# Kernel optimization log

Measured on AMD Instinct MI355X. Metric: run time of the kernel, lower is better.

The kernel has to match this reference:

```python
import jax, jax.numpy as jnp
import numpy as np

D = 256; H = 8; DH = D // H; L = 4; P = 4; NADJ = 4; DFF = 1024
SPATIAL_SHAPES = [(100, 134), (50, 67), (25, 34), (13, 17)]
LEVEL_START = [0, 13400, 16750, 17600]
LV = 17821
B, NQ, NP = 4, 100, 20


def layer_norm(x, g, b, eps=1e-5):
    m = x.mean(-1, keepdims=True)
    v = ((x - m) ** 2).mean(-1, keepdims=True)
    return (x - m) / jnp.sqrt(v + eps) * g + b


def mha(q, k, v, wi, bi, wo, bo):
    # q,k,v: [B', S, D]; torch nn.MultiheadAttention math (eval, no attn dropout effect on expectation pathway matters only in train)
    d = q.shape[-1]
    qp = q @ wi[:d].T + bi[:d]
    kp = k @ wi[d:2 * d].T + bi[d:2 * d]
    vp = v @ wi[2 * d:].T + bi[2 * d:]
    Bq, S, _ = qp.shape
    sp = lambda t: t.reshape(Bq, -1, H, DH).transpose(0, 2, 1, 3)
    att = jax.nn.softmax(jnp.einsum('bhqd,bhkd->bhqk', sp(qp), sp(kp)) / (DH ** 0.5), axis=-1)
    o = jnp.einsum('bhqk,bhkd->bhqd', att, sp(vp)).transpose(0, 2, 1, 3).reshape(Bq, S, d)
    return o @ wo.T + bo


def circonv(x, cw, cb, g, b, m, v):
    # Conv1d over point dim with circular padding NADJ, then BatchNorm1d (eval stats) + ReLU
    Bx, Nq, Np, d = x.shape
    t = x.reshape(Bx * Nq, Np, d).transpose(0, 2, 1)  # [B*Nq, C, Np]
    t = jnp.concatenate([t[..., -NADJ:], t, t[..., :NADJ]], axis=-1)
    t = jax.lax.conv_general_dilated(t, cw, (1,), 'VALID', dimension_numbers=('NCH', 'OIH', 'NCH'))
    t = t + cb[None, :, None]
    t = (t - m[None, :, None]) / jnp.sqrt(v[None, :, None] + 1e-5) * g[None, :, None] + b[None, :, None]
    t = jax.nn.relu(t)
    return t.transpose(0, 2, 1).reshape(Bx, Nq, Np, d)


def bilinear_gather(vflat, Hl, Wl, x, y):
    # vflat: [NB, Hl*Wl, DH]; x,y: [NB, S] pixel coords (align_corners=False, zero padding)
    x0 = jnp.floor(x); y0 = jnp.floor(y)
    lx = x - x0; ly = y - y0
    x0i = x0.astype(jnp.int32); y0i = y0.astype(jnp.int32)
    out = 0.
    for dy, wy in ((0, 1. - ly), (1, ly)):
        for dx, wx in ((0, 1. - lx), (1, lx)):
            xi = x0i + dx; yi = y0i + dy
            valid = (xi >= 0) & (xi < Wl) & (yi >= 0) & (yi < Hl)
            idx = jnp.clip(yi, 0, Hl - 1) * Wl + jnp.clip(xi, 0, Wl - 1)
            gs = jnp.take_along_axis(vflat, idx[..., None], axis=1)
            out = out + gs * (wx * wy * valid)[..., None]
    return out


def ms_deform_core(value, loc, weights):
    # value: [N, Lv, H, DH]; loc: [N, Lq, H, L, P, 2] in [0,1]; weights: [N, Lq, H, L, P]
    N, Lq = loc.shape[:2]
    out = jnp.zeros((N, Lq, H, DH), value.dtype)
    for lvl, (Hl, Wl) in enumerate(SPATIAL_SHAPES):
        s = LEVEL_START[lvl]
        vflat = value[:, s:s + Hl * Wl].transpose(0, 2, 1, 3).reshape(N * H, Hl * Wl, DH)
        g = 2. * loc[:, :, :, lvl] - 1.
        x = ((g[..., 0] + 1.) / 2.) * Wl - 0.5
        y = ((g[..., 1] + 1.) / 2.) * Hl - 0.5
        x = x.transpose(0, 2, 1, 3).reshape(N * H, Lq * P)
        y = y.transpose(0, 2, 1, 3).reshape(N * H, Lq * P)
        samp = bilinear_gather(vflat, Hl, Wl, x, y).reshape(N, H, Lq, P, DH)
        w = weights[:, :, :, lvl].transpose(0, 2, 1, 3)  # [N, H, Lq, P]
        out = out + jnp.einsum('nhqp,nhqpd->nqhd', w, samp)
    return out.reshape(N, Lq, D)


def ms_deform_attn(query, ref, src, so_w, so_b, aw_w, aw_b, vp_w, vp_b, op_w, op_b):
    N, Lq, _ = query.shape
    value = (src @ vp_w.T + vp_b).reshape(N, -1, H, DH)
    offsets = (query @ so_w.T + so_b).reshape(N, Lq, H, L, P, 2)
    aw = jax.nn.softmax((query @ aw_w.T + aw_b).reshape(N, Lq, H, L * P), -1).reshape(N, Lq, H, L, P)
    normalizer = jnp.array([[wl, hl] for hl, wl in SPATIAL_SHAPES], jnp.float32)  # [L, 2] (W, H)
    loc = ref[:, :, None, :, None, :] + offsets / normalizer[None, None, None, :, None, :]
    return ms_deform_core(value, loc, aw) @ op_w.T + op_b


def _forward(tgt, query_pos, query_pos_anchor, reference_points, src,
             ia_wi, ia_bi, ia_wo, ia_bo,
             cc_w, cc_b, bn_g, bn_b, bn_m, bn_v,
             ni_g, ni_b, mf_w, mf_b, nf_g, nf_b,
             in_wi, in_bi, in_wo, in_bo, nin_g, nin_b,
             so_w, so_b, aw_w, aw_b, vp_w, vp_b, op_w, op_b, nc_g, nc_b,
             l1_w, l1_b, l2_w, l2_b, n3_g, n3_b):
    Bx, Nq, Np, d = tgt.shape
    shortcut = tgt
    # intra-attention over points (DropPath/dropout are identity in eval)
    q = (tgt + query_pos).reshape(Bx * Nq, Np, d)
    t = mha(q, q, tgt.reshape(Bx * Nq, Np, d), ia_wi, ia_bi, ia_wo, ia_bo).reshape(Bx, Nq, Np, d)
    t_cc = circonv(shortcut + query_pos, cc_w, cc_b, bn_g, bn_b, bn_m, bn_v)
    tgt = shortcut + layer_norm(t + t_cc, ni_g, ni_b)
    tgt = tgt + layer_norm(tgt @ mf_w.T + mf_b, nf_g, nf_b)
    # inter-attention over instances
    ti = jnp.swapaxes(tgt, 1, 2)                                    # [B, Np, Nq, d]
    qi = jnp.swapaxes(tgt + query_pos_anchor, 1, 2).reshape(Bx * Np, Nq, d)
    t2 = mha(qi, qi, ti.reshape(Bx * Np, Nq, d), in_wi, in_bi, in_wo, in_bo).reshape(Bx, Np, Nq, d)
    ti = jnp.swapaxes(layer_norm(ti + t2, nin_g, nin_b), 1, 2)      # [B, Nq, Np, d]
    # deformable cross-attention
    qc = (ti + query_pos).reshape(Bx, Nq * Np, d)
    ref = reference_points.reshape(Bx, Nq * Np, L, 2)
    t2 = ms_deform_attn(qc, ref, src, so_w, so_b, aw_w, aw_b, vp_w, vp_b, op_w, op_b).reshape(Bx, Nq, Np, d)
    tgt = layer_norm(ti + t2, nc_g, nc_b)
    # FFN
    t2 = jax.nn.relu(tgt @ l1_w.T + l1_b) @ l2_w.T + l2_b
    return layer_norm(tgt + t2, n3_g, n3_b)


def setup_inputs() -> dict:
    ks = iter(jax.random.split(jax.random.key(0), 64))
    nx = lambda: next(ks)
    nrm = lambda shp, s=0.02: jax.random.normal(nx(), shp, jnp.float32) * s
    z = lambda shp: jnp.zeros(shp, jnp.float32)
    o = lambda shp: jnp.ones(shp, jnp.float32)
    inp = {
        'tgt': jax.random.normal(nx(), (B, NQ, NP, D), jnp.float32),
        'query_pos': jax.random.normal(nx(), (B, NQ, NP, D), jnp.float32),
        'query_pos_anchor': jax.random.normal(nx(), (B, NQ, NP, D), jnp.float32),
        'reference_points': jax.random.uniform(nx(), (B, NQ, NP, L, 2), jnp.float32),
        'src': jax.random.normal(nx(), (B, LV, D), jnp.float32),
        'src_spatial_shapes': jnp.array(SPATIAL_SHAPES, jnp.int32),
        'level_start_index': jnp.array(LEVEL_START, jnp.int32),
        'ia_wi': nrm((3 * D, D)), 'ia_bi': z((3 * D,)), 'ia_wo': nrm((D, D)), 'ia_bo': z((D,)),
        'cc_w': nrm((D, D, 2 * NADJ + 1), 0.01), 'cc_b': z((D,)),
        'bn_g': o((D,)), 'bn_b': z((D,)), 'bn_m': z((D,)), 'bn_v': o((D,)),
        'ni_g': o((D,)), 'ni_b': z((D,)),
        'mf_w': nrm((D, D)), 'mf_b': z((D,)),
        'nf_g': o((D,)), 'nf_b': z((D,)),
        'in_wi': nrm((3 * D, D)), 'in_bi': z((3 * D,)), 'in_wo': nrm((D, D)), 'in_bo': z((D,)),
        'nin_g': o((D,)), 'nin_b': z((D,)),
        'so_w': nrm((H * L * P * 2, D)), 'so_b': nrm((H * L * P * 2,), 0.1),
        'aw_w': nrm((H * L * P, D)), 'aw_b': z((H * L * P,)),
        'vp_w': nrm((D, D)), 'vp_b': z((D,)),
        'op_w': nrm((D, D)), 'op_b': z((D,)),
        'nc_g': o((D,)), 'nc_b': z((D,)),
        'l1_w': nrm((DFF, D)), 'l1_b': z((DFF,)),
        'l2_w': nrm((D, DFF)), 'l2_b': z((D,)),
        'n3_g': o((D,)), 'n3_b': z((D,)),
    }
    return inp


def reference(tgt, query_pos, query_pos_anchor, reference_points, src,
              src_spatial_shapes, level_start_index,
              ia_wi, ia_bi, ia_wo, ia_bo,
              cc_w, cc_b, bn_g, bn_b, bn_m, bn_v,
              ni_g, ni_b, mf_w, mf_b, nf_g, nf_b,
              in_wi, in_bi, in_wo, in_bo, nin_g, nin_b,
              so_w, so_b, aw_w, aw_b, vp_w, vp_b, op_w, op_b, nc_g, nc_b,
              l1_w, l1_b, l2_w, l2_b, n3_g, n3_b):
    # spatial shapes / level starts are compile-time constants (SPATIAL_SHAPES); the int tensors are accepted for API parity
    return _forward(tgt, query_pos, query_pos_anchor, reference_points, src,
                    ia_wi, ia_bi, ia_wo, ia_bo,
                    cc_w, cc_b, bn_g, bn_b, bn_m, bn_v,
                    ni_g, ni_b, mf_w, mf_b, nf_g, nf_b,
                    in_wi, in_bi, in_wo, in_bo, nin_g, nin_b,
                    so_w, so_b, aw_w, aw_b, vp_w, vp_b, op_w, op_b, nc_g, nc_b,
                    l1_w, l1_b, l2_w, l2_b, n3_g, n3_b)
```

## Files before the change

kernel.cpp:

```cpp
#include <hip/hip_runtime.h>
#include <cmath>

#define NTOK 8000
#define LV_TOT 17821

typedef __attribute__((ext_vector_type(8))) short short8;
typedef __attribute__((ext_vector_type(4))) float f32x4;

__device__ inline unsigned short f2bf(float f) {
  unsigned u = __float_as_uint(f);
  u += 0x7fffu + ((u >> 16) & 1u);
  return (unsigned short)(u >> 16);
}
__device__ inline short8 pack8(float4 a, float4 b) {
  short8 r;
  r[0] = (short)f2bf(a.x); r[1] = (short)f2bf(a.y);
  r[2] = (short)f2bf(a.z); r[3] = (short)f2bf(a.w);
  r[4] = (short)f2bf(b.x); r[5] = (short)f2bf(b.y);
  r[6] = (short)f2bf(b.z); r[7] = (short)f2bf(b.w);
  return r;
}
__device__ inline int swz(int row, int ib) {
  int s = ((ib >> 4) ^ (row & 3) ^ ((row >> 2) & 3)) & 3;
  return row * 64 + (s << 4) + (ib & 15);
}

__global__ __launch_bounds__(256) void add_kernel(const float* __restrict__ a,
                                                  const float* __restrict__ b,
                                                  float* __restrict__ o, int n4) {
  int i = blockIdx.x * 256 + threadIdx.x;
  if (i < n4) {
    float4 x = reinterpret_cast<const float4*>(a)[i];
    float4 y = reinterpret_cast<const float4*>(b)[i];
    float4 z; z.x = x.x + y.x; z.y = x.y + y.y; z.z = x.z + y.z; z.w = x.w + y.w;
    reinterpret_cast<float4*>(o)[i] = z;
  }
}

__global__ __launch_bounds__(256) void gemm_mfma_kernel(
    const float* __restrict__ A, const float* __restrict__ W,
    const float* __restrict__ s1, const float* __restrict__ s2,
    float* __restrict__ C, int M, int N, int K, int mode, int conv)
{
  __shared__ __align__(16) char lds[12288];
  char* ldsA = lds;
  char* ldsB = lds + 8192;

  const int tid = threadIdx.x;
  const int ar = tid >> 1, ac = (tid & 1) << 4;
  const int br = tid >> 2, bc = (tid & 3) << 3;
  const int arowg = blockIdx.y * 128 + ar;
  const int wrowg = blockIdx.x * 64 + br;
  const bool aval = arowg < M;
  int aseq = 0, anp = 0;
  if (conv) { aseq = arowg / 20; anp = arowg - aseq * 20; }
  const float* wsrc = W + (size_t)wrowg * K + bc;

  const int wv = tid >> 6, l = tid & 63, lr = l & 15, lk = l >> 4;

  f32x4 acc[2][4];
  #pragma unroll
  for (int m = 0; m < 2; ++m)
    #pragma unroll
    for (int n = 0; n < 4; ++n) acc[m][n] = (f32x4){0.f, 0.f, 0.f, 0.f};

  for (int k0 = 0; k0 < K; k0 += 32) {
    float4 a0 = make_float4(0.f,0.f,0.f,0.f), a1 = a0, a2 = a0, a3 = a0;
    if (aval) {
      const float* as;
      if (conv) {
        int kcol = k0 + ac, kt = kcol >> 8, c = kcol & 255;
        int sr = aseq * 20 + ((anp + kt + 16) % 20);
        as = A + (size_t)sr * 256 + c;
      } else {
        as = A + (size_t)arowg * K + k0 + ac;
      }
      a0 = *(const float4*)as;       a1 = *(const float4*)(as + 4);
      a2 = *(const float4*)(as + 8); a3 = *(const float4*)(as + 12);
    }
    float4 w0 = *(const float4*)(wsrc + k0);
    float4 w1 = *(const float4*)(wsrc + k0 + 4);
    __syncthreads();
    *(short8*)(ldsA + swz(ar, ac * 2))      = pack8(a0, a1);
    *(short8*)(ldsA + swz(ar, ac * 2 + 16)) = pack8(a2, a3);
    *(short8*)(ldsB + swz(br, bc * 2))      = pack8(w0, w1);
    __syncthreads();
    short8 af0 = *(short8*)(ldsA + swz(wv * 32 + lr,      lk * 16));
    short8 af1 = *(short8*)(ldsA + swz(wv * 32 + 16 + lr, lk * 16));
    #pragma unroll
    for (int n = 0; n < 4; ++n) {
      short8 bfr = *(short8*)(ldsB + swz(n * 16 + lr, lk * 16));
      acc[0][n] = __builtin_amdgcn_mfma_f32_16x16x32_bf16(af0, bfr, acc[0][n], 0, 0, 0);
      acc[1][n] = __builtin_amdgcn_mfma_f32_16x16x32_bf16(af1, bfr, acc[1][n], 0, 0, 0);
    }
  }
  #pragma unroll
  for (int n = 0; n < 4; ++n) {
    int gcol = blockIdx.x * 64 + n * 16 + lr;
    float sa = s1[gcol];
    float sb = (mode == 2) ? s2[gcol] : 0.f;
    #pragma unroll
    for (int m = 0; m < 2; ++m) {
      #pragma unroll
      for (int i = 0; i < 4; ++i) {
        int grow = blockIdx.y * 128 + wv * 32 + m * 16 + lk * 4 + i;
        if (grow < M) {
          float v = acc[m][n][i];
          v = (mode == 2) ? fmaxf(v * sa + sb, 0.f)
                          : (mode == 1 ? fmaxf(v + sa, 0.f) : v + sa);
          C[(size_t)grow * N + gcol] = v;
        }
      }
    }
  }
}

__global__ __launch_bounds__(256) void convw_kernel(const float* __restrict__ w,
                                                    float* __restrict__ w2) {
  int i = blockIdx.x * 256 + threadIdx.x;
  int o = i / 2304; int r = i - o * 2304;
  int k = r >> 8, c = r & 255;
  w2[i] = w[(size_t)o * 2304 + c * 9 + k];
}

__global__ __launch_bounds__(256) void bnfold_kernel(
    const float* __restrict__ cb, const float* __restrict__ g,
    const float* __restrict__ b,  const float* __restrict__ m,
    const float* __restrict__ v,  float* __restrict__ scale,
    float* __restrict__ shift) {
  int o = threadIdx.x;
  float s = g[o] * rsqrtf(v[o] + 1e-5f);
  scale[o] = s;
  shift[o] = (cb[o] - m[o]) * s + b[o];
}

__global__ __launch_bounds__(256) void ln_kernel(const float* __restrict__ x1,
    const float* __restrict__ x2, const float* __restrict__ x3,
    const float* __restrict__ g, const float* __restrict__ bta,
    float* __restrict__ out)
{
  int wid = threadIdx.x >> 6, lane = threadIdx.x & 63;
  size_t t = (size_t)blockIdx.x * 4 + wid;
  size_t base = t * 256 + (size_t)lane * 4;
  float4 v = *reinterpret_cast<const float4*>(x1 + base);
  if (x2) {
    float4 u = *reinterpret_cast<const float4*>(x2 + base);
    v.x += u.x; v.y += u.y; v.z += u.z; v.w += u.w;
  }
  float s  = v.x + v.y + v.z + v.w;
  float ss = v.x*v.x + v.y*v.y + v.z*v.z + v.w*v.w;
  #pragma unroll
  for (int off = 32; off; off >>= 1) {
    s  += __shfl_xor(s, off, 64);
    ss += __shfl_xor(ss, off, 64);
  }
  float mean = s * (1.0f / 256.0f);
  float var  = ss * (1.0f / 256.0f) - mean * mean;
  float rstd = rsqrtf(var + 1e-5f);
  float4 gv = *reinterpret_cast<const float4*>(g + lane * 4);
  float4 bv = *reinterpret_cast<const float4*>(bta + lane * 4);
  float4 o;
  o.x = (v.x - mean) * rstd * gv.x + bv.x;
  o.y = (v.y - mean) * rstd * gv.y + bv.y;
  o.z = (v.z - mean) * rstd * gv.z + bv.z;
  o.w = (v.w - mean) * rstd * gv.w + bv.w;
  if (x3) {
    float4 u = *reinterpret_cast<const float4*>(x3 + base);
    o.x += u.x; o.y += u.y; o.z += u.z; o.w += u.w;
  }
  *reinterpret_cast<float4*>(out + base) = o;
}

__global__ __launch_bounds__(256) void attn_intra_kernel(
    const float* __restrict__ qp, const float* __restrict__ kp,
    const float* __restrict__ vp, float* __restrict__ outb)
{
  __shared__ float Qs[20][257], Ks[20][257], Vs[20][257];
  int seq = blockIdx.x, t0 = seq * 20;
  for (int idx = threadIdx.x; idx < 20 * 256; idx += 256) {
    int r = idx >> 8, d = idx & 255;
    size_t g = (size_t)(t0 + r) * 256 + d;
    Qs[r][d] = qp[g]; Ks[r][d] = kp[g]; Vs[r][d] = vp[g];
  }
  __syncthreads();
  int h = threadIdx.x >> 5, i = threadIdx.x & 31;
  if (i < 20) {
    const float scale = 0.17677669529663687f;
    float s[20]; float m = -1e30f;
    #pragma unroll
    for (int j = 0; j < 20; ++j) {
      float a = 0.f;
      #pragma unroll
      for (int d = 0; d < 32; ++d) a += Qs[i][h*32+d] * Ks[j][h*32+d];
      a *= scale; s[j] = a; m = fmaxf(m, a);
    }
    float sum = 0.f;
    #pragma unroll
    for (int j = 0; j < 20; ++j) { s[j] = expf(s[j] - m); sum += s[j]; }
    float inv = 1.f / sum;
    #pragma unroll
    for (int d = 0; d < 32; ++d) {
      float o = 0.f;
      #pragma unroll
      for (int j = 0; j < 20; ++j) o += s[j] * Vs[j][h*32+d];
      outb[(size_t)(t0 + i) * 256 + h*32 + d] = o * inv;
    }
  }
}

__global__ __launch_bounds__(128) void attn_inter_kernel(
    const float* __restrict__ qp, const float* __restrict__ kp,
    const float* __restrict__ vp, float* __restrict__ outb)
{
  __shared__ float Ks[100][32], Vs[100][32];
  int blk = blockIdx.x;
  int h = blk & 7; int sp = blk >> 3; int np = sp % 20; int b = sp / 20;
  for (int idx = threadIdx.x; idx < 100 * 32; idx += 128) {
    int r = idx >> 5, d = idx & 31;
    size_t g = ((size_t)((b * 100 + r) * 20 + np)) * 256 + h*32 + d;
    Ks[r][d] = kp[g]; Vs[r][d] = vp[g];
  }
  __syncthreads();
  int i = threadIdx.x;
  if (i < 100) {
    size_t qbase = ((size_t)((b * 100 + i) * 20 + np)) * 256 + h*32;
    float q[32];
    #pragma unroll
    for (int d4 = 0; d4 < 8; ++d4) {
      float4 v = *reinterpret_cast<const float4*>(qp + qbase + d4*4);
      q[d4*4+0] = v.x; q[d4*4+1] = v.y; q[d4*4+2] = v.z; q[d4*4+3] = v.w;
    }
    const float scale = 0.17677669529663687f;
    float m = -1e30f, l = 0.f, o[32] = {};
    for (int j = 0; j < 100; ++j) {
      float s = 0.f;
      #pragma unroll
      for (int d = 0; d < 32; ++d) s += q[d] * Ks[j][d];
      s *= scale;
      float mn = fmaxf(m, s);
      float f = expf(m - mn), e = expf(s - mn);
      l = l * f + e;
      #pragma unroll
      for (int d = 0; d < 32; ++d) o[d] = o[d] * f + e * Vs[j][d];
      m = mn;
    }
    float inv = 1.f / l;
    #pragma unroll
    for (int d = 0; d < 32; ++d) outb[qbase + d] = o[d] * inv;
  }
}

__global__ __launch_bounds__(256) void deform_kernel(
    const float* __restrict__ value, const float* __restrict__ offs,
    const float* __restrict__ awl, const float* __restrict__ ref,
    float* __restrict__ outb)
{
  int t = blockIdx.x;
  int h = threadIdx.x >> 5, dh = threadIdx.x & 31;
  int b = t / 2000;
  float w[16]; float m = -1e30f;
  #pragma unroll
  for (int lp = 0; lp < 16; ++lp) {
    w[lp] = awl[(size_t)t * 128 + h * 16 + lp];
    m = fmaxf(m, w[lp]);
  }
  float sum = 0.f;
  #pragma unroll
  for (int lp = 0; lp < 16; ++lp) { w[lp] = expf(w[lp] - m); sum += w[lp]; }
  float inv = 1.f / sum;
  const int HLs[4] = {100, 50, 25, 13};
  const int WLs[4] = {134, 67, 34, 17};
  const int STs[4] = {0, 13400, 16750, 17600};
  float acc = 0.f;
  #pragma unroll
  for (int l = 0; l < 4; ++l) {
    const int Hl = HLs[l], Wl = WLs[l];
    const float* vb = value + ((size_t)(b * LV_TOT + STs[l])) * 256 + h*32 + dh;
    float rx = ref[(size_t)t * 8 + l * 2 + 0];
    float ry = ref[(size_t)t * 8 + l * 2 + 1];
    #pragma unroll
    for (int p = 0; p < 4; ++p) {
      size_t oi = (size_t)t * 256 + (size_t)(((h*4 + l)*4 + p)*2);
      float ox = offs[oi], oy = offs[oi + 1];
      float x = (rx + ox / (float)Wl) * (float)Wl - 0.5f;
      float y = (ry + oy / (float)Hl) * (float)Hl - 0.5f;
      float x0f = floorf(x), y0f = floorf(y);
      float lx = x - x0f, ly = y - y0f;
      int x0 = (int)x0f, y0 = (int)y0f;
      float wp = w[l*4 + p] * inv;
      float cw00 = (1.f-lx)*(1.f-ly)*wp, cw01 = lx*(1.f-ly)*wp;
      float cw10 = (1.f-lx)*ly*wp,       cw11 = lx*ly*wp;
      if (y0 >= 0 && y0 < Hl) {
        if (x0 >= 0 && x0 < Wl)         acc += cw00 * vb[(size_t)(y0*Wl + x0) * 256];
        if (x0+1 >= 0 && x0+1 < Wl)     acc += cw01 * vb[(size_t)(y0*Wl + x0+1) * 256];
      }
      if (y0+1 >= 0 && y0+1 < Hl) {
        if (x0 >= 0 && x0 < Wl)         acc += cw10 * vb[(size_t)((y0+1)*Wl + x0) * 256];
        if (x0+1 >= 0 && x0+1 < Wl)     acc += cw11 * vb[(size_t)((y0+1)*Wl + x0+1) * 256];
      }
    }
  }
  outb[(size_t)t * 256 + h*32 + dh] = acc;
}

extern "C" void kernel_launch(void* const* d_in, const int* in_sizes, int n_in,
                              void* d_out, int out_size, void* d_ws, size_t ws_size,
                              hipStream_t stream)
{
  const float* tgt  = (const float*)d_in[0];
  const float* qpos = (const float*)d_in[1];
  const float* qpa  = (const float*)d_in[2];
  const float* ref  = (const float*)d_in[3];
  const float* src  = (const float*)d_in[4];
  const float* ia_wi = (const float*)d_in[7];
  const float* ia_bi = (const float*)d_in[8];
  const float* ia_wo = (const float*)d_in[9];
  const float* ia_bo = (const float*)d_in[10];
  const float* cc_w  = (const float*)d_in[11];
  const float* cc_b  = (const float*)d_in[12];
  const float* bn_g  = (const float*)d_in[13];
  const float* bn_b  = (const float*)d_in[14];
  const float* bn_m  = (const float*)d_in[15];
  const float* bn_v  = (const float*)d_in[16];
  const float* ni_g  = (const float*)d_in[17];
  const float* ni_b  = (const float*)d_in[18];
  const float* mf_w  = (const float*)d_in[19];
  const float* mf_b  = (const float*)d_in[20];
  const float* nf_g  = (const float*)d_in[21];
  const float* nf_b  = (const float*)d_in[22];
  const float* in_wi = (const float*)d_in[23];
  const float* in_bi = (const float*)d_in[24];
  const float* in_wo = (const float*)d_in[25];
  const float* in_bo = (const float*)d_in[26];
  const float* nin_g = (const float*)d_in[27];
  const float* nin_b = (const float*)d_in[28];
  const float* so_w  = (const float*)d_in[29];
  const float* so_b  = (const float*)d_in[30];
  const float* aw_w  = (const float*)d_in[31];
  const float* aw_b  = (const float*)d_in[32];
  const float* vp_w  = (const float*)d_in[33];
  const float* vp_b  = (const float*)d_in[34];
  const float* op_w  = (const float*)d_in[35];
  const float* op_b  = (const float*)d_in[36];
  const float* nc_g  = (const float*)d_in[37];
  const float* nc_b  = (const float*)d_in[38];
  const float* l1_w  = (const float*)d_in[39];
  const float* l1_b  = (const float*)d_in[40];
  const float* l2_w  = (const float*)d_in[41];
  const float* l2_b  = (const float*)d_in[42];
  const float* n3_g  = (const float*)d_in[43];
  const float* n3_b  = (const float*)d_in[44];
  float* out = (float*)d_out;

  float* ws = (float*)d_ws;
  const size_t TD = (size_t)NTOK * 256;
  float* A   = ws;
  float* Bb  = ws + TD;
  float* Cc  = ws + 2*TD;
  float* Dd  = ws + 3*TD;
  float* Ee  = ws + 4*TD;
  float* V   = ws + 5*TD;
  float* W2  = V + (size_t)71284 * 256;
  float* bnscale = W2 + (size_t)256 * 2304;
  float* bnshift = bnscale + 256;
  float* Hbuf = V;

  dim3 blk(256);
  const int N4 = (int)(TD / 4);

  auto GEMM = [&](const float* Ain, const float* Win, const float* b1, const float* b2,
                  float* Cout, int M_, int N_, int K_, int mode, int conv) {
    dim3 g(N_ / 64, (M_ + 127) / 128);
    hipLaunchKernelGGL(gemm_mfma_kernel, g, blk, 0, stream,
                       Ain, Win, b1, b2, Cout, M_, N_, K_, mode, conv);
  };

  hipLaunchKernelGGL(add_kernel, dim3(2000), blk, 0, stream, tgt, qpos, A, N4);
  GEMM(A,   ia_wi,             ia_bi,       nullptr, Bb, NTOK, 256, 256, 0, 0);
  GEMM(A,   ia_wi + 256*256,   ia_bi + 256, nullptr, Cc, NTOK, 256, 256, 0, 0);
  GEMM(tgt, ia_wi + 512*256,   ia_bi + 512, nullptr, Dd, NTOK, 256, 256, 0, 0);
  hipLaunchKernelGGL(attn_intra_kernel, dim3(400), blk, 0, stream, Bb, Cc, Dd, Ee);
  GEMM(Ee,  ia_wo, ia_bo, nullptr, Bb, NTOK, 256, 256, 0, 0);

  hipLaunchKernelGGL(convw_kernel, dim3(2304), blk, 0, stream, cc_w, W2);
  hipLaunchKernelGGL(bnfold_kernel, dim3(1), blk, 0, stream,
                     cc_b, bn_g, bn_b, bn_m, bn_v, bnscale, bnshift);
  GEMM(A, W2, bnscale, bnshift, Cc, NTOK, 256, 2304, 2, 1);

  hipLaunchKernelGGL(ln_kernel, dim3(2000), blk, 0, stream, Bb, Cc, tgt, ni_g, ni_b, Dd);
  GEMM(Dd, mf_w, mf_b, nullptr, A, NTOK, 256, 256, 0, 0);
  hipLaunchKernelGGL(ln_kernel, dim3(2000), blk, 0, stream, A, (const float*)nullptr, Dd, nf_g, nf_b, Bb);

  hipLaunchKernelGGL(add_kernel, dim3(2000), blk, 0, stream, Bb, qpa, A, N4);
  GEMM(A,  in_wi,           in_bi,       nullptr, Cc, NTOK, 256, 256, 0, 0);
  GEMM(A,  in_wi + 256*256, in_bi + 256, nullptr, Dd, NTOK, 256, 256, 0, 0);
  GEMM(Bb, in_wi + 512*256, in_bi + 512, nullptr, Ee, NTOK, 256, 256, 0, 0);
  hipLaunchKernelGGL(attn_inter_kernel, dim3(640), dim3(128), 0, stream, Cc, Dd, Ee, A);
  GEMM(A, in_wo, in_bo, nullptr, Cc, NTOK, 256, 256, 0, 0);
  hipLaunchKernelGGL(ln_kernel, dim3(2000), blk, 0, stream, Bb, Cc, (const float*)nullptr, nin_g, nin_b, Dd);

  hipLaunchKernelGGL(add_kernel, dim3(2000), blk, 0, stream, Dd, qpos, A, N4);
  GEMM(src, vp_w, vp_b, nullptr, V, 4 * LV_TOT, 256, 256, 0, 0);
  GEMM(A, so_w, so_b, nullptr, Bb, NTOK, 256, 256, 0, 0);
  GEMM(A, aw_w, aw_b, nullptr, Cc, NTOK, 128, 256, 0, 0);
  hipLaunchKernelGGL(deform_kernel, dim3(NTOK), blk, 0, stream, V, Bb, Cc, ref, Ee);
  GEMM(Ee, op_w, op_b, nullptr, A, NTOK, 256, 256, 0, 0);
  hipLaunchKernelGGL(ln_kernel, dim3(2000), blk, 0, stream, Dd, A, (const float*)nullptr, nc_g, nc_b, Bb);

  GEMM(Bb, l1_w, l1_b, nullptr, Hbuf, NTOK, 1024, 256, 1, 0);
  GEMM(Hbuf, l2_w, l2_b, nullptr, A, NTOK, 256, 1024, 0, 0);
  hipLaunchKernelGGL(ln_kernel, dim3(2000), blk, 0, stream, Bb, A, (const float*)nullptr, n3_g, n3_b, out);
}
```

Measured before the change: 805.9 us.

## Fuse QKV projections, fold positional adds into GEMM loads, vectorize deform sampling

Merges the separate Q, K and V projection GEMMs into one GEMM with N=768, and merges the sampling-offset and attention-weight projections into one N=384 GEMM using a concatenated weight. The standalone add kernels are removed by adding the positional embedding during the GEMM A-tile load, applied only to column blocks below a limit. The deformable sampling kernel now runs four tokens per block, with each lane gathering float4 values. This cuts kernel launches and intermediate round trips, but the A operand is read twice when the add is active, and the new weight-concatenation kernel runs on every call.

```diff
diff --git a/kernel.cpp b/kernel.cpp
--- a/kernel.cpp
+++ b/kernel.cpp
@@ -25,22 +25,11 @@
   return row * 64 + (s << 4) + (ib & 15);
 }
 
-__global__ __launch_bounds__(256) void add_kernel(const float* __restrict__ a,
-                                                  const float* __restrict__ b,
-                                                  float* __restrict__ o, int n4) {
-  int i = blockIdx.x * 256 + threadIdx.x;
-  if (i < n4) {
-    float4 x = reinterpret_cast<const float4*>(a)[i];
-    float4 y = reinterpret_cast<const float4*>(b)[i];
-    float4 z; z.x = x.x + y.x; z.y = x.y + y.y; z.z = x.z + y.z; z.w = x.w + y.w;
-    reinterpret_cast<float4*>(o)[i] = z;
-  }
-}
-
 __global__ __launch_bounds__(256) void gemm_mfma_kernel(
-    const float* __restrict__ A, const float* __restrict__ W,
+    const float* __restrict__ A, const float* __restrict__ A2,
+    const float* __restrict__ W,
     const float* __restrict__ s1, const float* __restrict__ s2,
-    float* __restrict__ C, int M, int N, int K, int mode, int conv)
+    float* __restrict__ C, int M, int N, int K, int mode, int conv, int addLimit)
 {
   __shared__ __align__(16) char lds[12288];
   char* ldsA = lds;
@@ -52,6 +41,7 @@
   const int arowg = blockIdx.y * 128 + ar;
   const int wrowg = blockIdx.x * 64 + br;
   const bool aval = arowg < M;
+  const bool doadd = (A2 != nullptr) && ((int)blockIdx.x * 64 < addLimit);
   int aseq = 0, anp = 0;
   if (conv) { aseq = arowg / 20; anp = arowg - aseq * 20; }
   const float* wsrc = W + (size_t)wrowg * K + bc;
@@ -67,16 +57,26 @@
   for (int k0 = 0; k0 < K; k0 += 32) {
     float4 a0 = make_float4(0.f,0.f,0.f,0.f), a1 = a0, a2 = a0, a3 = a0;
     if (aval) {
-      const float* as;
+      size_t off;
       if (conv) {
         int kcol = k0 + ac, kt = kcol >> 8, c = kcol & 255;
         int sr = aseq * 20 + ((anp + kt + 16) % 20);
-        as = A + (size_t)sr * 256 + c;
+        off = (size_t)sr * 256 + c;
       } else {
-        as = A + (size_t)arowg * K + k0 + ac;
+        off = (size_t)arowg * K + k0 + ac;
       }
+      const float* as = A + off;
       a0 = *(const float4*)as;       a1 = *(const float4*)(as + 4);
       a2 = *(const float4*)(as + 8); a3 = *(const float4*)(as + 12);
+      if (doadd) {
+        const float* as2 = A2 + off;
+        float4 b0 = *(const float4*)as2;       float4 b1 = *(const float4*)(as2 + 4);
+        float4 b2 = *(const float4*)(as2 + 8); float4 b3 = *(const float4*)(as2 + 12);
+        a0.x+=b0.x; a0.y+=b0.y; a0.z+=b0.z; a0.w+=b0.w;
+        a1.x+=b1.x; a1.y+=b1.y; a1.z+=b1.z; a1.w+=b1.w;
+        a2.x+=b2.x; a2.y+=b2.y; a2.z+=b2.z; a2.w+=b2.w;
+        a3.x+=b3.x; a3.y+=b3.y; a3.z+=b3.z; a3.w+=b3.w;
+      }
     }
     float4 w0 = *(const float4*)(wsrc + k0);
     float4 w1 = *(const float4*)(wsrc + k0 + 4);
@@ -132,6 +132,15 @@
   float s = g[o] * rsqrtf(v[o] + 1e-5f);
   scale[o] = s;
   shift[o] = (cb[o] - m[o]) * s + b[o];
+}
+__global__ __launch_bounds__(256) void wcat_kernel(
+    const float* __restrict__ so_w, const float* __restrict__ so_b,
+    const float* __restrict__ aw_w, const float* __restrict__ aw_b,
+    float* __restrict__ wsb, float* __restrict__ bsb) {
+  int r = blockIdx.x, c = threadIdx.x;
+  wsb[(size_t)r * 256 + c] = (r < 256) ? so_w[(size_t)r * 256 + c]
+                                       : aw_w[(size_t)(r - 256) * 256 + c];
+  if (c == 0) bsb[r] = (r < 256) ? so_b[r] : aw_b[r - 256];
 }
 
 __global__ __launch_bounds__(256) void ln_kernel(const float* __restrict__ x1,
@@ -172,15 +181,14 @@
 }
 
 __global__ __launch_bounds__(256) void attn_intra_kernel(
-    const float* __restrict__ qp, const float* __restrict__ kp,
-    const float* __restrict__ vp, float* __restrict__ outb)
+    const float* __restrict__ qkv, float* __restrict__ outb)
 {
   __shared__ float Qs[20][257], Ks[20][257], Vs[20][257];
   int seq = blockIdx.x, t0 = seq * 20;
   for (int idx = threadIdx.x; idx < 20 * 256; idx += 256) {
     int r = idx >> 8, d = idx & 255;
-    size_t g = (size_t)(t0 + r) * 256 + d;
-    Qs[r][d] = qp[g]; Ks[r][d] = kp[g]; Vs[r][d] = vp[g];
+    size_t g = (size_t)(t0 + r) * 768 + d;
+    Qs[r][d] = qkv[g]; Ks[r][d] = qkv[g + 256]; Vs[r][d] = qkv[g + 512];
   }
   __syncthreads();
   int h = threadIdx.x >> 5, i = threadIdx.x & 31;
@@ -209,25 +217,25 @@
 }
 
 __global__ __launch_bounds__(128) void attn_inter_kernel(
-    const float* __restrict__ qp, const float* __restrict__ kp,
-    const float* __restrict__ vp, float* __restrict__ outb)
+    const float* __restrict__ qkv, float* __restrict__ outb)
 {
   __shared__ float Ks[100][32], Vs[100][32];
   int blk = blockIdx.x;
   int h = blk & 7; int sp = blk >> 3; int np = sp % 20; int b = sp / 20;
   for (int idx = threadIdx.x; idx < 100 * 32; idx += 128) {
     int r = idx >> 5, d = idx & 31;
-    size_t g = ((size_t)((b * 100 + r) * 20 + np)) * 256 + h*32 + d;
-    Ks[r][d] = kp[g]; Vs[r][d] = vp[g];
+    size_t g = ((size_t)((b * 100 + r) * 20 + np)) * 768 + h*32 + d;
+    Ks[r][d] = qkv[g + 256]; Vs[r][d] = qkv[g + 512];
   }
   __syncthreads();
   int i = threadIdx.x;
   if (i < 100) {
-    size_t qbase = ((size_t)((b * 100 + i) * 20 + np)) * 256 + h*32;
+    size_t tok = (size_t)(b * 100 + i) * 20 + np;
+    size_t qbase = tok * 768 + h*32;
     float q[32];
     #pragma unroll
     for (int d4 = 0; d4 < 8; ++d4) {
-      float4 v = *reinterpret_cast<const float4*>(qp + qbase + d4*4);
+      float4 v = *reinterpret_cast<const float4*>(qkv + qbase + d4*4);
       q[d4*4+0] = v.x; q[d4*4+1] = v.y; q[d4*4+2] = v.z; q[d4*4+3] = v.w;
     }
     const float scale = 0.17677669529663687f;
@@ -246,24 +254,23 @@
     }
     float inv = 1.f / l;
     #pragma unroll
-    for (int d = 0; d < 32; ++d) outb[qbase + d] = o[d] * inv;
+    for (int d = 0; d < 32; ++d) outb[tok * 256 + h*32 + d] = o[d] * inv;
   }
 }
 
 __global__ __launch_bounds__(256) void deform_kernel(
-    const float* __restrict__ value, const float* __restrict__ offs,
-    const float* __restrict__ awl, const float* __restrict__ ref,
-    float* __restrict__ outb)
-{
-  int t = blockIdx.x;
-  int h = threadIdx.x >> 5, dh = threadIdx.x & 31;
+    const float* __restrict__ value, const float* __restrict__ oa,
+    const float* __restrict__ ref, float* __restrict__ outb)
+{
+  int t = blockIdx.x * 4 + (threadIdx.x >> 6);
+  int lane = threadIdx.x & 63;
+  int h = lane >> 3, q4 = (lane & 7) << 2;
   int b = t / 2000;
+  const float* awp  = oa + (size_t)t * 384 + 256 + h * 16;
+  const float* offp = oa + (size_t)t * 384 + h * 32;
   float w[16]; float m = -1e30f;
   #pragma unroll
-  for (int lp = 0; lp < 16; ++lp) {
-    w[lp] = awl[(size_t)t * 128 + h * 16 + lp];
-    m = fmaxf(m, w[lp]);
-  }
+  for (int lp = 0; lp < 16; ++lp) { w[lp] = awp[lp]; m = fmaxf(m, w[lp]); }
   float sum = 0.f;
   #pragma unroll
   for (int lp = 0; lp < 16; ++lp) { w[lp] = expf(w[lp] - m); sum += w[lp]; }
@@ -271,17 +278,16 @@
   const int HLs[4] = {100, 50, 25, 13};
   const int WLs[4] = {134, 67, 34, 17};
   const int STs[4] = {0, 13400, 16750, 17600};
-  float acc = 0.f;
+  float4 acc = make_float4(0.f, 0.f, 0.f, 0.f);
   #pragma unroll
   for (int l = 0; l < 4; ++l) {
     const int Hl = HLs[l], Wl = WLs[l];
-    const float* vb = value + ((size_t)(b * LV_TOT + STs[l])) * 256 + h*32 + dh;
+    const float* vb = value + ((size_t)(b * LV_TOT + STs[l])) * 256 + h*32 + q4;
     float rx = ref[(size_t)t * 8 + l * 2 + 0];
     float ry = ref[(size_t)t * 8 + l * 2 + 1];
     #pragma unroll
     for (int p = 0; p < 4; ++p) {
-      size_t oi = (size_t)t * 256 + (size_t)(((h*4 + l)*4 + p)*2);
-      float ox = offs[oi], oy = offs[oi + 1];
+      float ox = offp[(l*4 + p)*2], oy = offp[(l*4 + p)*2 + 1];
       float x = (rx + ox / (float)Wl) * (float)Wl - 0.5f;
       float y = (ry + oy / (float)Hl) * (float)Hl - 0.5f;
       float x0f = floorf(x), y0f = floorf(y);
@@ -290,17 +296,19 @@
       float wp = w[l*4 + p] * inv;
       float cw00 = (1.f-lx)*(1.f-ly)*wp, cw01 = lx*(1.f-ly)*wp;
       float cw10 = (1.f-lx)*ly*wp,       cw11 = lx*ly*wp;
-      if (y0 >= 0 && y0 < Hl) {
-        if (x0 >= 0 && x0 < Wl)         acc += cw00 * vb[(size_t)(y0*Wl + x0) * 256];
-        if (x0+1 >= 0 && x0+1 < Wl)     acc += cw01 * vb[(size_t)(y0*Wl + x0+1) * 256];
-      }
-      if (y0+1 >= 0 && y0+1 < Hl) {
-        if (x0 >= 0 && x0 < Wl)         acc += cw10 * vb[(size_t)((y0+1)*Wl + x0) * 256];
-        if (x0+1 >= 0 && x0+1 < Wl)     acc += cw11 * vb[(size_t)((y0+1)*Wl + x0+1) * 256];
-      }
-    }
-  }
-  outb[(size_t)t * 256 + h*32 + dh] = acc;
+      bool yv0 = (y0 >= 0) & (y0 < Hl), yv1 = (y0+1 >= 0) & (y0+1 < Hl);
+      bool xv0 = (x0 >= 0) & (x0 < Wl), xv1 = (x0+1 >= 0) & (x0+1 < Wl);
+      if (yv0 & xv0) { float4 v = *(const float4*)(vb + (size_t)(y0*Wl + x0) * 256);
+        acc.x += cw00*v.x; acc.y += cw00*v.y; acc.z += cw00*v.z; acc.w += cw00*v.w; }
+      if (yv0 & xv1) { float4 v = *(const float4*)(vb + (size_t)(y0*Wl + x0+1) * 256);
+        acc.x += cw01*v.x; acc.y += cw01*v.y; acc.z += cw01*v.z; acc.w += cw01*v.w; }
+      if (yv1 & xv0) { float4 v = *(const float4*)(vb + (size_t)((y0+1)*Wl + x0) * 256);
+        acc.x += cw10*v.x; acc.y += cw10*v.y; acc.z += cw10*v.z; acc.w += cw10*v.w; }
+      if (yv1 & xv1) { float4 v = *(const float4*)(vb + (size_t)((y0+1)*Wl + x0+1) * 256);
+        acc.x += cw11*v.x; acc.y += cw11*v.y; acc.z += cw11*v.z; acc.w += cw11*v.w; }
+    }
+  }
+  *(float4*)(outb + (size_t)t * 256 + h*32 + q4) = acc;
 }
 
 extern "C" void kernel_launch(void* const* d_in, const int* in_sizes, int n_in,
@@ -353,61 +361,54 @@
   float* out = (float*)d_out;
 
   float* ws = (float*)d_ws;
-  const size_t TD = (size_t)NTOK * 256;
-  float* A   = ws;
-  float* Bb  = ws + TD;
-  float* Cc  = ws + 2*TD;
-  float* Dd  = ws + 3*TD;
-  float* Ee  = ws + 4*TD;
-  float* V   = ws + 5*TD;
-  float* W2  = V + (size_t)71284 * 256;
-  float* bnscale = W2 + (size_t)256 * 2304;
+  const size_t TD  = (size_t)NTOK * 256;
+  const size_t QVs = (size_t)71284 * 256;
+  float* QV = ws;
+  float* T1 = ws + QVs;
+  float* T2 = T1 + TD;
+  float* T3 = T2 + TD;
+  float* T4 = T3 + TD;
+  float* W2 = T4 + TD;
+  float* WSB = W2 + (size_t)256 * 2304;
+  float* BSB = WSB + (size_t)384 * 256;
+  float* bnscale = BSB + 384;
   float* bnshift = bnscale + 256;
-  float* Hbuf = V;
 
   dim3 blk(256);
-  const int N4 = (int)(TD / 4);
-
-  auto GEMM = [&](const float* Ain, const float* Win, const float* b1, const float* b2,
-                  float* Cout, int M_, int N_, int K_, int mode, int conv) {
+  auto GEMM = [&](const float* Ain, const float* Aadd, const float* Win,
+                  const float* b1, const float* b2, float* Cout,
+                  int M_, int N_, int K_, int mode, int conv, int addLim) {
     dim3 g(N_ / 64, (M_ + 127) / 128);
     hipLaunchKernelGGL(gemm_mfma_kernel, g, blk, 0, stream,
-                       Ain, Win, b1, b2, Cout, M_, N_, K_, mode, conv);
+                       Ain, Aadd, Win, b1, b2, Cout, M_, N_, K_, mode, conv, addLim);
   };
 
-  hipLaunchKernelGGL(add_kernel, dim3(2000), blk, 0, stream, tgt, qpos, A, N4);
-  GEMM(A,   ia_wi,             ia_bi,       nullptr, Bb, NTOK, 256, 256, 0, 0);
-  GEMM(A,   ia_wi + 256*256,   ia_bi + 256, nullptr, Cc, NTOK, 256, 256, 0, 0);
-  GEMM(tgt, ia_wi + 512*256,   ia_bi + 512, nullptr, Dd, NTOK, 256, 256, 0, 0);
-  hipLaunchKernelGGL(attn_intra_kernel, dim3(400), blk, 0, stream, Bb, Cc, Dd, Ee);
-  GEMM(Ee,  ia_wo, ia_bo, nullptr, Bb, NTOK, 256, 256, 0, 0);
+  GEMM(tgt, qpos, ia_wi, ia_bi, nullptr, QV, NTOK, 768, 256, 0, 0, 512);
+  hipLaunchKernelGGL(attn_intra_kernel, dim3(400), blk, 0, stream, QV, T1);
+  GEMM(T1, nullptr, ia_wo, ia_bo, nullptr, T2, NTOK, 256, 256, 0, 0, 0);
 
   hipLaunchKernelGGL(convw_kernel, dim3(2304), blk, 0, stream, cc_w, W2);
   hipLaunchKernelGGL(bnfold_kernel, dim3(1), blk, 0, stream,
                      cc_b, bn_g, bn_b, bn_m, bn_v, bnscale, bnshift);
-  GEMM(A, W2, bnscale, bnshift, Cc, NTOK, 256, 2304, 2, 1);
-
-  hipLaunchKernelGGL(ln_kernel, dim3(2000), blk, 0, stream, Bb, Cc, tgt, ni_g, ni_b, Dd);
-  GEMM(Dd, mf_w, mf_b, nullptr, A, NTOK, 256, 256, 0, 0);
-  hipLaunchKernelGGL(ln_kernel, dim3(2000), blk, 0, stream, A, (const float*)nullptr, Dd, nf_g, nf_b, Bb);
-
-  hipLaunchKernelGGL(add_kernel, dim3(2000), blk, 0, stream, Bb, qpa, A, N4);
-  GEMM(A,  in_wi,           in_bi,       nullptr, Cc, NTOK, 256, 256, 0, 0);
-  GEMM(A,  in_wi + 256*256, in_bi + 256, nullptr, Dd, NTOK, 256, 256, 0, 0);
-  GEMM(Bb, in_wi + 512*256, in_bi + 512, nullptr, Ee, NTOK, 256, 256, 0, 0);
-  hipLaunchKernelGGL(attn_inter_kernel, dim3(640), dim3(128), 0, stream, Cc, Dd, Ee, A);
-  GEMM(A, in_wo, in_bo, nullptr, Cc, NTOK, 256, 256, 0, 0);
-  hipLaunchKernelGGL(ln_kernel, dim3(2000), blk, 0, stream, Bb, Cc, (const float*)nullptr, nin_g, nin_b, Dd);
-
-  hipLaunchKernelGGL(add_kernel, dim3(2000), blk, 0, stream, Dd, qpos, A, N4);
-  GEMM(src, vp_w, vp_b, nullptr, V, 4 * LV_TOT, 256, 256, 0, 0);
-  GEMM(A, so_w, so_b, nullptr, Bb, NTOK, 256, 256, 0, 0);
-  GEMM(A, aw_w, aw_b, nullptr, Cc, NTOK, 128, 256, 0, 0);
-  hipLaunchKernelGGL(deform_kernel, dim3(NTOK), blk, 0, stream, V, Bb, Cc, ref, Ee);
-  GEMM(Ee, op_w, op_b, nullptr, A, NTOK, 256, 256, 0, 0);
-  hipLaunchKernelGGL(ln_kernel, dim3(2000), blk, 0, stream, Dd, A, (const float*)nullptr, nc_g, nc_b, Bb);
-
-  GEMM(Bb, l1_w, l1_b, nullptr, Hbuf, NTOK, 1024, 256, 1, 0);
-  GEMM(Hbuf, l2_w, l2_b, nullptr, A, NTOK, 256, 1024, 0, 0);
-  hipLaunchKernelGGL(ln_kernel, dim3(2000), blk, 0, stream, Bb, A, (const float*)nullptr, n3_g, n3_b, out);
-}
+  GEMM(tgt, qpos, W2, bnscale, bnshift, T3, NTOK, 256, 2304, 2, 1, 256);
+
+  hipLaunchKernelGGL(ln_kernel, dim3(2000), blk, 0, stream, T2, T3, tgt, ni_g, ni_b, T4);
+  GEMM(T4, nullptr, mf_w, mf_b, nullptr, T1, NTOK, 256, 256, 0, 0, 0);
+  hipLaunchKernelGGL(ln_kernel, dim3(2000), blk, 0, stream, T1, (const float*)nullptr, T4, nf_g, nf_b, T2);
+
+  GEMM(T2, qpa, in_wi, in_bi, nullptr, QV, NTOK, 768, 256, 0, 0, 512);
+  hipLaunchKernelGGL(attn_inter_kernel, dim3(640), dim3(128), 0, stream, QV, T1);
+  GEMM(T1, nullptr, in_wo, in_bo, nullptr, T3, NTOK, 256, 256, 0, 0, 0);
+  hipLaunchKernelGGL(ln_kernel, dim3(2000), blk, 0, stream, T2, T3, (const float*)nullptr, nin_g, nin_b, T4);
+
+  hipLaunchKernelGGL(wcat_kernel, dim3(384), blk, 0, stream, so_w, so_b, aw_w, aw_b, WSB, BSB);
+  GEMM(src, nullptr, vp_w, vp_b, nullptr, QV, 4 * LV_TOT, 256, 256, 0, 0, 0);
+  GEMM(T4, qpos, WSB, BSB, nullptr, T1, NTOK, 384, 256, 0, 0, 384);
+  hipLaunchKernelGGL(deform_kernel, dim3(2000), blk, 0, stream, QV, T1, ref, T3);
+  GEMM(T3, nullptr, op_w, op_b, nullptr, T2, NTOK, 256, 256, 0, 0, 0);
+  hipLaunchKernelGGL(ln_kernel, dim3(2000), blk, 0, stream, T4, T2, (const float*)nullptr, nc_g, nc_b, T1);
+
+  GEMM(T1, nullptr, l1_w, l1_b, nullptr, QV, NTOK, 1024, 256, 1, 0, 0);
+  GEMM(QV, nullptr, l2_w, l2_b, nullptr, T2, NTOK, 256, 1024, 0, 0, 0);
+  hipLaunchKernelGGL(ln_kernel, dim3(2000), blk, 0, stream, T1, T2, (const float*)nullptr, n3_g, n3_b, out);
+}
```

New measurement: 731.6 us. -9.2%, faster.
